# Kernel optimization log

Hardware: AMD Instinct MI355X
Metric: run time of the kernel (lower is better)

The kernel has to match this reference:

```python
import jax, jax.numpy as jnp
import numpy as np

B = 2097152  # batch
H = 2        # GRU hidden size


def _gru_cell(x, h, w_ih, w_hh, b_ih, b_hh):
    # torch.nn.GRUCell math. w_ih: [3H, I], w_hh: [3H, H]
    gi = x @ w_ih.T + b_ih  # [B, 3H]
    gh = h @ w_hh.T + b_hh  # [B, 3H]
    i_r, i_z, i_n = jnp.split(gi, 3, axis=-1)
    h_r, h_z, h_n = jnp.split(gh, 3, axis=-1)
    r = jax.nn.sigmoid(i_r + h_r)
    z = jax.nn.sigmoid(i_z + h_z)
    n = jnp.tanh(i_n + r * h_n)
    return (1.0 - z) * n + z * h


def setup_inputs() -> dict:
    key = jax.random.key(0)
    ks = jax.random.split(key, 14)
    f32 = jnp.float32
    inp = {
        "x": jax.random.normal(ks[0], (B, 18), dtype=f32),
        # r_up: GRUCell(2, 2)
        "w_ih_up": 0.3 * jax.random.normal(ks[1], (3 * H, 2), dtype=f32),
        "w_hh_up": 0.3 * jax.random.normal(ks[2], (3 * H, H), dtype=f32),
        "b_ih_up": 0.1 * jax.random.normal(ks[3], (3 * H,), dtype=f32),
        "b_hh_up": 0.1 * jax.random.normal(ks[4], (3 * H,), dtype=f32),
        # fc_obs: Linear(6, 2)
        "w_obs": 0.3 * jax.random.normal(ks[5], (2, 6), dtype=f32),
        "b_obs": 0.1 * jax.random.normal(ks[6], (2,), dtype=f32),
        # r_down: GRUCell(2, 2)
        "w_ih_dn": 0.3 * jax.random.normal(ks[7], (3 * H, 2), dtype=f32),
        "w_hh_dn": 0.3 * jax.random.normal(ks[8], (3 * H, H), dtype=f32),
        "b_ih_dn": 0.1 * jax.random.normal(ks[9], (3 * H,), dtype=f32),
        "b_hh_dn": 0.1 * jax.random.normal(ks[10], (3 * H,), dtype=f32),
        # fc_out: Linear(2, 1)
        "w_out": 0.3 * jax.random.normal(ks[11], (1, H), dtype=f32),
        "b_out": 0.1 * jax.random.normal(ks[12], (1,), dtype=f32),
    }
    return inp


def reference(x, w_ih_up, w_hh_up, b_ih_up, b_hh_up, w_obs, b_obs,
              w_ih_dn, w_hh_dn, b_ih_dn, b_hh_dn, w_out, b_out):
    obs = x[:, :4]            # [B, 4]
    j = x[:, 4:11]            # [B, 7]
    jd = x[:, 11:]            # [B, 7]
    jcat = jnp.stack([j, jd], axis=1)  # [B, 2, 7]

    # upward recurrence over the 7 joints, reversed order
    h = jnp.zeros((x.shape[0], H), dtype=x.dtype)
    h_up = []
    for i in reversed(range(7)):
        h = _gru_cell(jcat[:, :, i], h, w_ih_up, w_hh_up, b_ih_up, b_hh_up)
        h_up.append(h)

    # fuse observation into the hidden state
    h = jnp.concatenate([obs, h], axis=1) @ w_obs.T + b_obs  # [B, 2]

    # downward recurrence, emitting one action per joint
    acts = []
    for i in range(7):
        h = _gru_cell(h_up[i], h, w_ih_dn, w_hh_dn, b_ih_dn, b_hh_dn)
        acts.append(h @ w_out.T + b_out)  # [B, 1]
    return jnp.concatenate(acts, axis=1)  # [B, 7]
```

## Files before the change

kernel.cpp:

```cpp
#include <hip/hip_runtime.h>


using v2f = __attribute__((ext_vector_type(2))) float;

__device__ __forceinline__ float fexp2(float x) { return __builtin_amdgcn_exp2f(x); }
__device__ __forceinline__ float frcp(float x)  { return __builtin_amdgcn_rcpf(x); }

struct Cell {
    v2f wr0, wr1, ur0, ur1, br;
    v2f wz0, wz1, uz0, uz1, bz;
    v2f wn0, wn1, bni;
    v2f un0, un1, bnh;
};

__global__ void prep_kernel(
    const float* __restrict__ w_ih_up, const float* __restrict__ w_hh_up,
    const float* __restrict__ b_ih_up, const float* __restrict__ b_hh_up,
    const float* __restrict__ w_obs,   const float* __restrict__ b_obs,
    const float* __restrict__ w_ih_dn, const float* __restrict__ w_hh_dn,
    const float* __restrict__ b_ih_dn, const float* __restrict__ b_hh_dn,
    const float* __restrict__ w_out,   const float* __restrict__ b_out,
    float* __restrict__ ws)
{
    if (threadIdx.x != 0 || blockIdx.x != 0) return;
    const float s1 = -1.4426950408889634f;
    const float s2 =  2.8853900817779268f;
    #pragma unroll
    for (int c = 0; c < 2; ++c) {
        const float* wi = c ? w_ih_dn : w_ih_up;
        const float* wh = c ? w_hh_dn : w_hh_up;
        const float* bi = c ? b_ih_dn : b_ih_up;
        const float* bh = c ? b_hh_dn : b_hh_up;
        float* o = ws + c * 64;
        o[0] = s1*wi[0]; o[1] = s1*wi[2];  o[2] = s1*wi[1]; o[3] = s1*wi[3];
        o[4] = s1*wh[0]; o[5] = s1*wh[2];  o[6] = s1*wh[1]; o[7] = s1*wh[3];
        o[8] = s1*(bi[0]+bh[0]); o[9] = s1*(bi[1]+bh[1]);
        o[10] = s1*wi[4]; o[11] = s1*wi[6]; o[12] = s1*wi[5]; o[13] = s1*wi[7];
        o[14] = s1*wh[4]; o[15] = s1*wh[6]; o[16] = s1*wh[5]; o[17] = s1*wh[7];
        o[18] = s1*(bi[2]+bh[2]); o[19] = s1*(bi[3]+bh[3]);
        o[20] = s2*wi[8]; o[21] = s2*wi[10]; o[22] = s2*wi[9]; o[23] = s2*wi[11];
        o[24] = s2*bi[4]; o[25] = s2*bi[5];
        o[26] = s2*wh[8]; o[27] = s2*wh[10]; o[28] = s2*wh[9]; o[29] = s2*wh[11];
        o[30] = s2*bh[4]; o[31] = s2*bh[5];
    }
    #pragma unroll
    for (int i = 0; i < 12; ++i) ws[128 + i] = w_obs[i];
    ws[140] = b_obs[0]; ws[141] = b_obs[1];
    ws[142] = w_out[0]; ws[143] = w_out[1];
    ws[144] = b_out[0];
}

__device__ __forceinline__ void gru(const Cell& c, float x0, float x1, v2f& h) {
    v2f gr = c.br + c.wr0 * x0 + c.wr1 * x1 + c.ur0 * h.x + c.ur1 * h.y;
    v2f gz = c.bz + c.wz0 * x0 + c.wz1 * x1 + c.uz0 * h.x + c.uz1 * h.y;
    v2f dr = (v2f){1.0f + fexp2(gr.x), 1.0f + fexp2(gr.y)};
    v2f dz = (v2f){1.0f + fexp2(gz.x), 1.0f + fexp2(gz.y)};
    float invr = frcp(dr.x * dr.y);
    v2f r = invr * (v2f){dr.y, dr.x};
    v2f gi = c.bni + c.wn0 * x0 + c.wn1 * x1;
    v2f gh = c.bnh + c.un0 * h.x + c.un1 * h.y;
    v2f a  = gi + r * gh;
    v2f da = (v2f){1.0f + fexp2(a.x), 1.0f + fexp2(a.y)};
    float m = -2.0f * frcp(da.x * da.y);
    v2f n = (v2f){fmaf(m, da.y, 1.0f), fmaf(m, da.x, 1.0f)};
    float invz = frcp(dz.x * dz.y);
    v2f z = invz * (v2f){dz.y, dz.x};
    h = n + z * (h - n);
}

__device__ __forceinline__ void row_chain(
    const Cell& up, const Cell& dn, const float* __restrict__ W,
    const float* row, float acts[7])
{
    v2f h = (v2f){0.0f, 0.0f};
    v2f hu[7];
    #pragma unroll
    for (int k = 0; k < 7; ++k) {
        const int i = 6 - k;
        gru(up, row[4 + i], row[11 + i], h);
        hu[k] = h;
    }
    {
        v2f t = (v2f){W[140], W[141]};
        #pragma unroll
        for (int c = 0; c < 4; ++c)
            t += (v2f){W[128 + c], W[134 + c]} * row[c];
        t += (v2f){W[132], W[138]} * h.x;
        t += (v2f){W[133], W[139]} * h.y;
        h = t;
    }
    const float wo0 = W[142], wo1 = W[143], bo = W[144];
    #pragma unroll
    for (int k = 0; k < 7; ++k) {
        gru(dn, hu[k].x, hu[k].y, h);
        acts[k] = fmaf(wo0, h.x, fmaf(wo1, h.y, bo));
    }
}

__device__ __forceinline__ void dma_tile(const float* __restrict__ x,
                                         size_t t, float* in_lds, int lane)
{
    const char* g = reinterpret_cast<const char*>(x) + t * 4608;
    char* l = reinterpret_cast<char*>(in_lds);
    #pragma unroll
    for (int k = 0; k < 4; ++k) {
        __builtin_amdgcn_global_load_lds(
            (const __attribute__((address_space(1))) void*)(g + k * 1024 + lane * 16),
            (__attribute__((address_space(3))) void*)(l + k * 1024), 16, 0, 0);
    }
    #pragma unroll
    for (int c = 0; c < 2; ++c) {
        __builtin_amdgcn_global_load_lds(
            (const __attribute__((address_space(1))) void*)(g + 4096 + c * 256 + lane * 4),
            (__attribute__((address_space(3))) void*)(l + 4096 + c * 256), 4, 0, 0);
    }
}

__global__ __launch_bounds__(256) void recpolicy_kernel(
    const float* __restrict__ x, const float* __restrict__ W,
    float* __restrict__ out, int n)
{
    __shared__ float lds[4 * 1600];
    const int tid  = threadIdx.x;
    const int wid  = tid >> 6;
    const int lane = tid & 63;
    float* inb  = lds + wid * 1600;
    float* outb = inb + 1152;

    const Cell up = *reinterpret_cast<const Cell*>(W);
    const Cell dn = *reinterpret_cast<const Cell*>(W + 64);

    const int NT = n >> 6;
    const int NW = gridDim.x << 2;
    int t = (blockIdx.x << 2) | wid;

    if (t < NT) {
        dma_tile(x, (size_t)t, inb, lane);
        while (true) {
            asm volatile("s_waitcnt vmcnt(0)" ::: "memory");
            __builtin_amdgcn_sched_barrier(0);

            float rowv[18];
            {
                const float2* rp = reinterpret_cast<const float2*>(inb + lane * 18);
                #pragma unroll
                for (int i = 0; i < 9; ++i) {
                    float2 v = rp[i];
                    rowv[2 * i] = v.x; rowv[2 * i + 1] = v.y;
                }
            }
            asm volatile("s_waitcnt lgkmcnt(0)" ::: "memory");
            __builtin_amdgcn_sched_barrier(0);

            const int tn = t + NW;
            if (tn < NT) dma_tile(x, (size_t)tn, inb, lane);

            float acts[7];
            row_chain(up, dn, W, rowv, acts);

            #pragma unroll
            for (int k = 0; k < 7; ++k) outb[lane * 7 + k] = acts[k];
            {
                const float4* so = reinterpret_cast<const float4*>(outb);
                float4* dsto = reinterpret_cast<float4*>(out) + (size_t)t * 112;
                dsto[lane] = so[lane];
                if (lane < 48) dsto[lane + 64] = so[lane + 64];
            }

            if (tn >= NT) break;
            t = tn;
        }
    }

    const int tail0 = NT << 6;
    if (blockIdx.x == 0 && wid == 0 && tail0 < n) {
        const int rg = tail0 + lane;
        if (rg < n) {
            float rowl[18];
            #pragma unroll
            for (int i = 0; i < 18; ++i) rowl[i] = x[(size_t)rg * 18 + i];
            float acts[7];
            row_chain(up, dn, W, rowl, acts);
            #pragma unroll
            for (int k = 0; k < 7; ++k) out[(size_t)rg * 7 + k] = acts[k];
        }
    }
}

extern "C" void kernel_launch(void* const* d_in, const int* in_sizes, int n_in,
                              void* d_out, int out_size, void* d_ws, size_t ws_size,
                              hipStream_t stream) {
    const float* x       = (const float*)d_in[0];
    const float* w_ih_up = (const float*)d_in[1];
    const float* w_hh_up = (const float*)d_in[2];
    const float* b_ih_up = (const float*)d_in[3];
    const float* b_hh_up = (const float*)d_in[4];
    const float* w_obs   = (const float*)d_in[5];
    const float* b_obs   = (const float*)d_in[6];
    const float* w_ih_dn = (const float*)d_in[7];
    const float* w_hh_dn = (const float*)d_in[8];
    const float* b_ih_dn = (const float*)d_in[9];
    const float* b_hh_dn = (const float*)d_in[10];
    const float* w_out   = (const float*)d_in[11];
    const float* b_out   = (const float*)d_in[12];
    float* out = (float*)d_out;
    float* ws  = (float*)d_ws;

    prep_kernel<<<1, 64, 0, stream>>>(
        w_ih_up, w_hh_up, b_ih_up, b_hh_up, w_obs, b_obs,
        w_ih_dn, w_hh_dn, b_ih_dn, b_hh_dn, w_out, b_out, ws);

    const int n = in_sizes[0] / 18;
    recpolicy_kernel<<<1536, 256, 0, stream>>>(x, ws, out, n);
}
```

Baseline: 54.73 us.

## Use producer warp with double-buffered 448-row tiles per block

Restructures the kernel into a warp-specialized design: one wave per 512-thread block issues async global-to-LDS loads of a 448-row tile into a double buffer while seven compute waves process the previous tile. Per-wave private 64-row tiles with self-prefetch are replaced by block-level tiles with __syncthreads handoff. This aims to hide load latency behind compute. In exchange, one wave in eight does no arithmetic, every tile step adds a block barrier, and the grid shrinks to 512 blocks.

```diff
diff --git a/kernel.cpp b/kernel.cpp
--- a/kernel.cpp
+++ b/kernel.cpp
@@ -97,84 +97,88 @@
     }
 }
 
-__device__ __forceinline__ void dma_tile(const float* __restrict__ x,
-                                         size_t t, float* in_lds, int lane)
-{
-    const char* g = reinterpret_cast<const char*>(x) + t * 4608;
-    char* l = reinterpret_cast<char*>(in_lds);
-    #pragma unroll
-    for (int k = 0; k < 4; ++k) {
+__device__ __forceinline__ void dma_tile448(const float* __restrict__ x,
+                                            long t, float* dstlds, int lane)
+{
+    const char* g = reinterpret_cast<const char*>(x) + t * 32256;
+    char* l = reinterpret_cast<char*>(dstlds);
+    #pragma unroll
+    for (int k = 0; k < 31; ++k)
         __builtin_amdgcn_global_load_lds(
             (const __attribute__((address_space(1))) void*)(g + k * 1024 + lane * 16),
             (__attribute__((address_space(3))) void*)(l + k * 1024), 16, 0, 0);
-    }
-    #pragma unroll
-    for (int c = 0; c < 2; ++c) {
+    #pragma unroll
+    for (int c = 0; c < 2; ++c)
         __builtin_amdgcn_global_load_lds(
-            (const __attribute__((address_space(1))) void*)(g + 4096 + c * 256 + lane * 4),
-            (__attribute__((address_space(3))) void*)(l + 4096 + c * 256), 4, 0, 0);
-    }
-}
-
-__global__ __launch_bounds__(256) void recpolicy_kernel(
+            (const __attribute__((address_space(1))) void*)(g + 31744 + c * 256 + lane * 4),
+            (__attribute__((address_space(3))) void*)(l + 31744 + c * 256), 4, 0, 0);
+}
+
+#define TILE_ROWS 448
+#define TILE_F    8064
+
+__global__ __launch_bounds__(512) void recpolicy_kernel(
     const float* __restrict__ x, const float* __restrict__ W,
     float* __restrict__ out, int n)
 {
-    __shared__ float lds[4 * 1600];
+    __shared__ float lds[2 * TILE_F + 7 * 448];
     const int tid  = threadIdx.x;
     const int wid  = tid >> 6;
     const int lane = tid & 63;
-    float* inb  = lds + wid * 1600;
-    float* outb = inb + 1152;
 
     const Cell up = *reinterpret_cast<const Cell*>(W);
     const Cell dn = *reinterpret_cast<const Cell*>(W + 64);
 
-    const int NT = n >> 6;
-    const int NW = gridDim.x << 2;
-    int t = (blockIdx.x << 2) | wid;
+    const int NT = n / TILE_ROWS;
+    const int S  = gridDim.x;
+    int t = blockIdx.x;
 
     if (t < NT) {
-        dma_tile(x, (size_t)t, inb, lane);
+        int cur = 0;
+        if (wid == 0) dma_tile448(x, (long)t, lds, lane);
         while (true) {
-            asm volatile("s_waitcnt vmcnt(0)" ::: "memory");
-            __builtin_amdgcn_sched_barrier(0);
-
-            float rowv[18];
-            {
-                const float2* rp = reinterpret_cast<const float2*>(inb + lane * 18);
+            if (wid == 0) asm volatile("s_waitcnt vmcnt(0)" ::: "memory");
+            __syncthreads();
+
+            const int tn = t + S;
+            if (wid == 0) {
+                if (tn < NT)
+                    dma_tile448(x, (long)tn, lds + (cur ^ 1) * TILE_F, lane);
+            } else {
+                const int c = wid - 1;
+                const float* row = lds + cur * TILE_F + (c * 64 + lane) * 18;
+                float rowv[18];
+                {
+                    const float2* rp = reinterpret_cast<const float2*>(row);
+                    #pragma unroll
+                    for (int i = 0; i < 9; ++i) {
+                        float2 v = rp[i];
+                        rowv[2 * i] = v.x; rowv[2 * i + 1] = v.y;
+                    }
+                }
+                float acts[7];
+                row_chain(up, dn, W, rowv, acts);
+
+                float* outb = lds + 2 * TILE_F + c * 448;
                 #pragma unroll
-                for (int i = 0; i < 9; ++i) {
-                    float2 v = rp[i];
-                    rowv[2 * i] = v.x; rowv[2 * i + 1] = v.y;
+                for (int k = 0; k < 7; ++k) outb[lane * 7 + k] = acts[k];
+                {
+                    const float4* so = reinterpret_cast<const float4*>(outb);
+                    float4* dsto = reinterpret_cast<float4*>(out)
+                                 + (size_t)t * 784 + c * 112;
+                    dsto[lane] = so[lane];
+                    if (lane < 48) dsto[lane + 64] = so[lane + 64];
                 }
             }
-            asm volatile("s_waitcnt lgkmcnt(0)" ::: "memory");
-            __builtin_amdgcn_sched_barrier(0);
-
-            const int tn = t + NW;
-            if (tn < NT) dma_tile(x, (size_t)tn, inb, lane);
-
-            float acts[7];
-            row_chain(up, dn, W, rowv, acts);
-
-            #pragma unroll
-            for (int k = 0; k < 7; ++k) outb[lane * 7 + k] = acts[k];
-            {
-                const float4* so = reinterpret_cast<const float4*>(outb);
-                float4* dsto = reinterpret_cast<float4*>(out) + (size_t)t * 112;
-                dsto[lane] = so[lane];
-                if (lane < 48) dsto[lane + 64] = so[lane + 64];
-            }
 
             if (tn >= NT) break;
-            t = tn;
+            t = tn; cur ^= 1;
         }
     }
 
-    const int tail0 = NT << 6;
-    if (blockIdx.x == 0 && wid == 0 && tail0 < n) {
-        const int rg = tail0 + lane;
+    const int tail0 = NT * TILE_ROWS;
+    if (blockIdx.x == 0 && wid >= 1 && tail0 < n) {
+        const int rg = tail0 + (wid - 1) * 64 + lane;
         if (rg < n) {
             float rowl[18];
             #pragma unroll
@@ -211,5 +215,5 @@
         w_ih_dn, w_hh_dn, b_ih_dn, b_hh_dn, w_out, b_out, ws);
 
     const int n = in_sizes[0] / 18;
-    recpolicy_kernel<<<1536, 256, 0, stream>>>(x, ws, out, n);
-}
+    recpolicy_kernel<<<512, 512, 0, stream>>>(x, ws, out, n);
+}
```

Measured after the change: 59.36 us. 1.08x slower.
